# Optimization experiments

Measured on AMD Instinct MI355X. Metric: run time of the kernel, lower is better.

Reference implementation:

```python
import jax, jax.numpy as jnp
import numpy as np

N = 201        # nodes (100 visual + 100 audio + 1 text)
E = 40200      # directed edges (before self loops)
IN_CH = 1024
HD_CH = 1024
OUT_CH = 1024
HEADS = 8
C1 = HD_CH // HEADS   # 128 per-head channels, layer 1
C2 = OUT_CH // HEADS  # 128 per-head channels, layer 2
NUM_CLS = 2
NEG_SLOPE = 0.2


def setup_inputs() -> dict:
    key = jax.random.key(0)
    ks = jax.random.split(key, 16)

    def lin(k, out_d, in_d):
        return jax.random.normal(k, (out_d, in_d), jnp.float32) * (1.0 / np.sqrt(in_d))

    x = jax.random.normal(ks[0], (1, N, IN_CH), jnp.float32)
    edgeIds = jax.random.randint(ks[1], (2, E), 0, N, jnp.int64)
    return {
        "x": x,
        "edgeIds": edgeIds,
        # GATv2 layer 1
        "W1l": lin(ks[2], HEADS * C1, IN_CH), "b1l": jnp.zeros((HEADS * C1,), jnp.float32),
        "W1r": lin(ks[3], HEADS * C1, IN_CH), "b1r": jnp.zeros((HEADS * C1,), jnp.float32),
        "att1": jax.random.normal(ks[4], (HEADS, C1), jnp.float32) * (1.0 / np.sqrt(C1)),
        "bias1": jnp.zeros((HEADS * C1,), jnp.float32),
        # GATv2 layer 2
        "W2l": lin(ks[5], HEADS * C2, HD_CH), "b2l": jnp.zeros((HEADS * C2,), jnp.float32),
        "W2r": lin(ks[6], HEADS * C2, HD_CH), "b2r": jnp.zeros((HEADS * C2,), jnp.float32),
        "att2": jax.random.normal(ks[7], (HEADS, C2), jnp.float32) * (1.0 / np.sqrt(C2)),
        "bias2": jnp.zeros((HEADS * C2,), jnp.float32),
        # classifier
        "clfW": lin(ks[8], NUM_CLS, OUT_CH),
        "clfb": jnp.zeros((NUM_CLS,), jnp.float32),
    }


def _gatv2(x, src, dst, Wl, bl, Wr, br, att, bias, heads, ch):
    # x: [N, in_ch]; src/dst: [E'] (self loops included)
    n = x.shape[0]
    xl = (x @ Wl.T + bl).reshape(n, heads, ch)  # source transform
    xr = (x @ Wr.T + br).reshape(n, heads, ch)  # target transform
    # per-edge GATv2 score: a^T LeakyReLU(xl_j + xr_i)
    e = jax.nn.leaky_relu(xl[src] + xr[dst], NEG_SLOPE)   # [E', H, C]
    score = jnp.einsum("ehc,hc->eh", e, att)              # [E', H]
    # segment softmax over destination nodes (PyG convention)
    smax = jax.ops.segment_max(score, dst, num_segments=n)     # [N, H]
    ex = jnp.exp(score - smax[dst])                            # [E', H]
    denom = jax.ops.segment_sum(ex, dst, num_segments=n)       # [N, H]
    alpha = ex / (denom[dst] + 1e-16)                          # [E', H]
    out = jax.ops.segment_sum(alpha[:, :, None] * xl[src], dst, num_segments=n)
    return out.reshape(n, heads * ch) + bias


def reference(x, edgeIds, W1l, b1l, W1r, b1r, att1, bias1,
              W2l, b2l, W2r, b2r, att2, bias2, clfW, clfb):
    xs = jnp.squeeze(x, axis=0)  # [N, inChl]
    n = xs.shape[0]
    # add_self_loops=True (GATv2Conv default)
    loops = jnp.arange(n, dtype=edgeIds.dtype)
    src = jnp.concatenate([edgeIds[0], loops])
    dst = jnp.concatenate([edgeIds[1], loops])

    h = _gatv2(xs, src, dst, W1l, b1l, W1r, b1r, att1, bias1, HEADS, C1)
    h = jax.nn.relu(h)
    h = _gatv2(h, src, dst, W2l, b2l, W2r, b2r, att2, bias2, HEADS, C2)

    h = h[None]  # [1, N, outChl]
    # fuse_average: mean of visual (0:100), audio (100:200), text (node 200)
    avg = (jnp.mean(h[:, :100], axis=1) + jnp.mean(h[:, 100:200], axis=1) + h[:, 200]) / 3.0
    return avg @ clfW.T + clfb  # [1, numCls]
```

## Files before the change

kernel.cpp:

```cpp
#include <hip/hip_runtime.h>
#include <hip/hip_bf16.h>

#define HEADS 8
#define MPAD  208
#define KPAD  224
#define HROWS 112
#define NB    208

typedef __attribute__((ext_vector_type(8))) short short8v;
typedef __attribute__((ext_vector_type(4))) float float4v;

static __device__ __forceinline__ unsigned short f2bf(float f) {
    unsigned int u = __float_as_uint(f);
    u += 0x7FFF + ((u >> 16) & 1);
    return (unsigned short)(u >> 16);
}
static __device__ __forceinline__ float bf2f(unsigned short h) {
    return __uint_as_float(((unsigned int)h) << 16);
}

__global__ void k_mzero(int* M) {
    int i = blockIdx.x * 1024 + threadIdx.x;
    if (i < MPAD * KPAD) M[i] = 0;
}

__global__ void k_mcount(const int* __restrict__ srcA, const int* __restrict__ dstA,
                         int E, int N, int* __restrict__ M) {
    int e = blockIdx.x * 256 + threadIdx.x;
    if (e < E + N) {
        int d = (e < E) ? dstA[e] : (e - E);
        int s = (e < E) ? srcA[e] : (e - E);
        atomicAdd(&M[d * KPAD + s], 1);
    }
}

template<int MODE>
__global__ __launch_bounds__(256)
void k_gemm_mfma(const float* __restrict__ Xf, const unsigned short* __restrict__ Apl,
                 const float* __restrict__ Wl, const float* __restrict__ bl,
                 const float* __restrict__ Wr, const float* __restrict__ br,
                 unsigned short* __restrict__ outT) {
    __shared__ short lA[2 * HROWS * 40];
    __shared__ short lB[2 * 16 * 40];

    int tx = threadIdx.x;
    int panel = blockIdx.x >> 1;
    int half  = blockIdx.x & 1;
    int row0  = half * HROWS;
    int ntiles = half ? 6 : 7;
    int wv = tx >> 6, lane = tx & 63;
    int colpan = (panel & 63) * 16;
    const float* Wbase = (panel < 64) ? Wl : Wr;

    int gX[4], lX[4], rowv[4];
    #pragma unroll
    for (int j = 0; j < 4; ++j) {
        int idx = tx + 256 * j;
        if (MODE == 0) {
            int r = idx >> 3, seg = idx & 7;
            rowv[j] = row0 + r;
            gX[j] = (row0 + r) * 1024 + seg * 4;
            lX[j] = r * 40 + seg * 4;
        } else {
            int p = (idx >= 448);
            int rem = idx - p * 448;
            int r = rem >> 2, seg = rem & 3;
            rowv[j] = row0 + r;
            gX[j] = (p * MPAD + row0 + r) * 1024 + seg * 8;
            lX[j] = p * (HROWS * 40) + r * 40 + seg * 8;
        }
    }
    int wcol = tx >> 3, wseg = tx & 7;
    size_t goffW = (size_t)(colpan + wcol) * 1024 + wseg * 4;

    float4  af[4];
    short8v ap[4];
    float4  wreg;

    auto loadChunk = [&](int k0) {
        #pragma unroll
        for (int j = 0; j < 3; ++j) {
            if (MODE == 0) {
                af[j] = (rowv[j] < 201) ? *(const float4*)&Xf[gX[j] + k0]
                                        : make_float4(0.f, 0.f, 0.f, 0.f);
            } else {
                ap[j] = (rowv[j] < 201) ? *(const short8v*)&Apl[gX[j] + k0]
                                        : short8v{0,0,0,0,0,0,0,0};
            }
        }
        if (tx < 128) {
            if (MODE == 0) {
                af[3] = (rowv[3] < 201) ? *(const float4*)&Xf[gX[3] + k0]
                                        : make_float4(0.f, 0.f, 0.f, 0.f);
            } else {
                ap[3] = (rowv[3] < 201) ? *(const short8v*)&Apl[gX[3] + k0]
                                        : short8v{0,0,0,0,0,0,0,0};
            }
            wreg = *(const float4*)&Wbase[goffW + k0];
        }
    };
    auto storeSeg = [&](int j) {
        if (MODE == 0) {
            ushort4 hi, lo;
            hi.x = f2bf(af[j].x); lo.x = f2bf(af[j].x - bf2f(hi.x));
            hi.y = f2bf(af[j].y); lo.y = f2bf(af[j].y - bf2f(hi.y));
            hi.z = f2bf(af[j].z); lo.z = f2bf(af[j].z - bf2f(hi.z));
            hi.w = f2bf(af[j].w); lo.w = f2bf(af[j].w - bf2f(hi.w));
            *(ushort4*)&lA[lX[j]]              = hi;
            *(ushort4*)&lA[HROWS * 40 + lX[j]] = lo;
        } else {
            *(short8v*)&lA[lX[j]] = ap[j];
        }
    };
    auto storeChunk = [&]() {
        #pragma unroll
        for (int j = 0; j < 3; ++j) storeSeg(j);
        if (tx < 128) {
            storeSeg(3);
            ushort4 hi, lo;
            hi.x = f2bf(wreg.x); lo.x = f2bf(wreg.x - bf2f(hi.x));
            hi.y = f2bf(wreg.y); lo.y = f2bf(wreg.y - bf2f(hi.y));
            hi.z = f2bf(wreg.z); lo.z = f2bf(wreg.z - bf2f(hi.z));
            hi.w = f2bf(wreg.w); lo.w = f2bf(wreg.w - bf2f(hi.w));
            *(ushort4*)&lB[wcol * 40 + wseg * 4]        = hi;
            *(ushort4*)&lB[(16 + wcol) * 40 + wseg * 4] = lo;
        }
    };

    float4v acc[2] = {};
    int row16 = lane & 15;
    int k8    = (lane >> 4) * 8;

    loadChunk(0);
    for (int c = 0; c < 32; ++c) {
        __syncthreads();
        storeChunk();
        __syncthreads();
        if (c < 31) loadChunk((c + 1) * 32);
        short8v bh  = *(const short8v*)&lB[row16 * 40 + k8];
        short8v blo = *(const short8v*)&lB[(16 + row16) * 40 + k8];
        #pragma unroll
        for (int i = 0; i < 2; ++i) {
            int t = wv + 4 * i;
            if (t < ntiles) {
                short8v ah = *(const short8v*)&lA[(t * 16 + row16) * 40 + k8];
                short8v al = *(const short8v*)&lA[HROWS * 40 + (t * 16 + row16) * 40 + k8];
                acc[i] = __builtin_amdgcn_mfma_f32_16x16x32_bf16(ah, bh,  acc[i], 0, 0, 0);
                acc[i] = __builtin_amdgcn_mfma_f32_16x16x32_bf16(al, bh,  acc[i], 0, 0, 0);
                acc[i] = __builtin_amdgcn_mfma_f32_16x16x32_bf16(ah, blo, acc[i], 0, 0, 0);
            }
        }
    }

    int colg = panel * 16 + row16;
    float bias_val = ((panel < 64) ? bl : br)[colpan + row16];
    unsigned short* Th = outT;
    unsigned short* Tl = outT + (size_t)2048 * KPAD;
    #pragma unroll
    for (int i = 0; i < 2; ++i) {
        int t = wv + 4 * i;
        if (t < ntiles) {
            int rowb = row0 + t * 16 + (lane >> 4) * 4;
            ushort4 hi, lo;
            float v0 = acc[i][0] + bias_val, v1 = acc[i][1] + bias_val;
            float v2 = acc[i][2] + bias_val, v3 = acc[i][3] + bias_val;
            hi.x = f2bf(v0); lo.x = f2bf(v0 - bf2f(hi.x));
            hi.y = f2bf(v1); lo.y = f2bf(v1 - bf2f(hi.y));
            hi.z = f2bf(v2); lo.z = f2bf(v2 - bf2f(hi.z));
            hi.w = f2bf(v3); lo.w = f2bf(v3 - bf2f(hi.w));
            *(ushort4*)&Th[(size_t)colg * KPAD + rowb] = hi;
            *(ushort4*)&Tl[(size_t)colg * KPAD + rowb] = lo;
        }
    }
}

template<int LAYER1>
__global__ __launch_bounds__(256)
void k_score(const unsigned short* __restrict__ outT,
             const float* __restrict__ att, const float* __restrict__ bias,
             const int* __restrict__ M,
             unsigned short* __restrict__ hpl,
             const float* __restrict__ clfW, float* __restrict__ part) {
    __shared__ float xrt[8 * 128];
    __shared__ float a_l[128], a4_l[128];
    __shared__ float axr_l[8];
    __shared__ float Sm[8][256];
    __shared__ float smax_l[8], inv_l[8];
    __shared__ unsigned short aP[2][16][232];
    __shared__ float ps[4][2];

    int tx = threadIdx.x;
    int bid = blockIdx.x;
    int h = bid & 7, dt = bid >> 3;
    int w = tx >> 6, lane = tx & 63;
    const unsigned short* Th = outT;
    const unsigned short* Tl = outT + (size_t)2048 * KPAD;

    if (tx < 128) { float a = att[h * 128 + tx]; a_l[tx] = a; a4_l[tx] = 0.4f * a; }
    #pragma unroll
    for (int k = 0; k < 4; ++k) {
        int idx = tx + 256 * k;
        int c = idx >> 3, j = idx & 7;
        size_t o = (size_t)(1024 + h * 128 + c) * KPAD + dt * 8 + j;
        xrt[j * 128 + c] = bf2f(Th[o]) + bf2f(Tl[o]);
    }
    for (int k = tx; k < 2 * 8 * 232; k += 256) {
        int pl = k / (8 * 232), rem = k % (8 * 232);
        aP[pl][8 + rem / 232][rem % 232] = 0;
    }
    __syncthreads();
    if (tx < 64) {
        int j = tx >> 3, seg = tx & 7;
        float s = 0.f;
        for (int c = seg * 16; c < seg * 16 + 16; ++c) s += a_l[c] * xrt[j * 128 + c];
        s += __shfl_xor(s, 1, 64);
        s += __shfl_xor(s, 2, 64);
        s += __shfl_xor(s, 4, 64);
        if (seg == 0) axr_l[j] = s;
    }
    __syncthreads();

    float sc[8] = {};
    float axl = 0.f;
    {
        size_t base = (size_t)(h * 128) * KPAD + tx;
        for (int c = 0; c < 128; ++c) {
            size_t o = base + (size_t)c * KPAD;
            float xv = bf2f(Th[o]) + bf2f(Tl[o]);
            axl = fmaf(a_l[c], xv, axl);
            #pragma unroll
            for (int j = 0; j < 8; ++j) {
                float t0 = xv + xrt[j * 128 + c];
                sc[j] = fmaf(a4_l[c], fabsf(t0), sc[j]);
            }
        }
    }
    float cnt[8];
    #pragma unroll
    for (int j = 0; j < 8; ++j) {
        float c_ = 0.f;
        if (tx < KPAD) c_ = (float)M[(dt * 8 + j) * KPAD + tx];
        cnt[j] = c_;
        sc[j] = 0.6f * (axl + axr_l[j]) + sc[j];
        Sm[j][tx] = (c_ > 0.f) ? sc[j] : -__builtin_huge_valf();
    }
    __syncthreads();
    #pragma unroll
    for (int rr = 0; rr < 2; ++rr) {
        int j = w * 2 + rr;
        float v = fmaxf(fmaxf(Sm[j][lane], Sm[j][lane + 64]),
                        fmaxf(Sm[j][lane + 128], Sm[j][lane + 192]));
        #pragma unroll
        for (int hop = 1; hop <= 32; hop <<= 1) v = fmaxf(v, __shfl_xor(v, hop, 64));
        if (lane == 0) smax_l[j] = v;
    }
    __syncthreads();
    float pj[8];
    #pragma unroll
    for (int j = 0; j < 8; ++j) {
        float p = (cnt[j] > 0.f) ? cnt[j] * __expf(sc[j] - smax_l[j]) : 0.f;
        pj[j] = p;
        Sm[j][tx] = p;
    }
    __syncthreads();
    #pragma unroll
    for (int rr = 0; rr < 2; ++rr) {
        int j = w * 2 + rr;
        float v = Sm[j][lane] + Sm[j][lane + 64] + Sm[j][lane + 128] + Sm[j][lane + 192];
        #pragma unroll
        for (int hop = 1; hop <= 32; hop <<= 1) v += __shfl_xor(v, hop, 64);
        if (lane == 0) inv_l[j] = 1.f / (v + 1e-16f);
    }
    __syncthreads();
    if (tx < KPAD) {
        #pragma unroll
        for (int j = 0; j < 8; ++j) {
            float a = pj[j] * inv_l[j];
            unsigned short hi = f2bf(a);
            unsigned short lo = f2bf(a - bf2f(hi));
            aP[0][j][tx] = hi;
            aP[1][j][tx] = lo;
        }
    }
    __syncthreads();

    float4v acc[2] = {};
    int row16 = lane & 15;
    int k8 = (lane >> 4) * 8;
    for (int kc = 0; kc < 7; ++kc) {
        short8v Ah = *(const short8v*)&aP[0][row16][kc * 32 + k8];
        short8v Al = *(const short8v*)&aP[1][row16][kc * 32 + k8];
        #pragma unroll
        for (int cf = 0; cf < 2; ++cf) {
            int c_abs = h * 128 + w * 32 + cf * 16 + row16;
            size_t o = (size_t)c_abs * KPAD + kc * 32 + k8;
            short8v Bh = *(const short8v*)&Th[o];
            short8v Bl = *(const short8v*)&Tl[o];
            acc[cf] = __builtin_amdgcn_mfma_f32_16x16x32_bf16(Ah, Bh, acc[cf], 0, 0, 0);
            acc[cf] = __builtin_amdgcn_mfma_f32_16x16x32_bf16(Al, Bh, acc[cf], 0, 0, 0);
            acc[cf] = __builtin_amdgcn_mfma_f32_16x16x32_bf16(Ah, Bl, acc[cf], 0, 0, 0);
        }
    }

    int r = (lane >> 4) * 4;
    if (LAYER1) {
        if (r < 8) {
            #pragma unroll
            for (int cf = 0; cf < 2; ++cf) {
                int c_abs = h * 128 + w * 32 + cf * 16 + (lane & 15);
                float bv = bias[c_abs];
                #pragma unroll
                for (int j = 0; j < 4; ++j) {
                    int d = dt * 8 + r + j;
                    float val = fmaxf(acc[cf][j] + bv, 0.f);
                    unsigned short hi = f2bf(val);
                    unsigned short lo = f2bf(val - bf2f(hi));
                    hpl[(size_t)d * 1024 + c_abs]          = hi;
                    hpl[(size_t)(MPAD + d) * 1024 + c_abs] = lo;
                }
            }
        }
    } else {
        float p0 = 0.f, p1 = 0.f;
        if (r < 8) {
            #pragma unroll
            for (int cf = 0; cf < 2; ++cf) {
                int c_abs = h * 128 + w * 32 + cf * 16 + (lane & 15);
                float bv = bias[c_abs];
                float c0 = clfW[c_abs], c1 = clfW[1024 + c_abs];
                #pragma unroll
                for (int j = 0; j < 4; ++j) {
                    int d = dt * 8 + r + j;
                    if (d < 201) {
                        float val = acc[cf][j] + bv;
                        float wgt = (d == 200) ? (1.f / 3.f) : (1.f / 300.f);
                        p0 += wgt * val * c0;
                        p1 += wgt * val * c1;
                    }
                }
            }
        }
        #pragma unroll
        for (int hop = 1; hop <= 32; hop <<= 1) {
            p0 += __shfl_xor(p0, hop, 64);
            p1 += __shfl_xor(p1, hop, 64);
        }
        if (lane == 0) { ps[w][0] = p0; ps[w][1] = p1; }
        __syncthreads();
        if (tx == 0) {
            part[bid]      = ps[0][0] + ps[1][0] + ps[2][0] + ps[3][0];
            part[NB + bid] = ps[0][1] + ps[1][1] + ps[2][1] + ps[3][1];
        }
    }
}

__global__ __launch_bounds__(256)
void k_fin(const float* __restrict__ part, const float* __restrict__ clfb,
           float* __restrict__ outp) {
    int t = threadIdx.x;
    float s0 = (t < NB) ? part[t] : 0.f;
    float s1 = (t < NB) ? part[NB + t] : 0.f;
    __shared__ float r0[256], r1[256];
    r0[t] = s0; r1[t] = s1;
    __syncthreads();
    for (int off = 128; off > 0; off >>= 1) {
        if (t < off) { r0[t] += r0[t + off]; r1[t] += r1[t + off]; }
        __syncthreads();
    }
    if (t == 0) { outp[0] = r0[0] + clfb[0]; outp[1] = r0[0] * 0.f + r1[0] + clfb[1]; }
}

extern "C" void kernel_launch(void* const* d_in, const int* in_sizes, int n_in,
                              void* d_out, int out_size, void* d_ws, size_t ws_size,
                              hipStream_t stream) {
    const float* x     = (const float*)d_in[0];
    const int*   eids  = (const int*)d_in[1];
    const float* W1l   = (const float*)d_in[2];
    const float* b1l   = (const float*)d_in[3];
    const float* W1r   = (const float*)d_in[4];
    const float* b1r   = (const float*)d_in[5];
    const float* att1  = (const float*)d_in[6];
    const float* bias1 = (const float*)d_in[7];
    const float* W2l   = (const float*)d_in[8];
    const float* b2l   = (const float*)d_in[9];
    const float* W2r   = (const float*)d_in[10];
    const float* b2r   = (const float*)d_in[11];
    const float* att2  = (const float*)d_in[12];
    const float* bias2 = (const float*)d_in[13];
    const float* clfW  = (const float*)d_in[14];
    const float* clfb  = (const float*)d_in[15];
    float* outp = (float*)d_out;

    int N = in_sizes[0] / 1024;
    int E = in_sizes[1] / 2;
    int tot = E + N;

    char* wsp = (char*)d_ws;
    int* M = (int*)wsp;                         wsp += (size_t)MPAD * KPAD * 4;
    unsigned short* outT1 = (unsigned short*)wsp; wsp += (size_t)2 * 2048 * KPAD * 2;
    unsigned short* hpl   = (unsigned short*)wsp; wsp += (size_t)2 * MPAD * 1024 * 2;
    unsigned short* outT2 = (unsigned short*)wsp; wsp += (size_t)2 * 2048 * KPAD * 2;
    float* part = (float*)wsp;                   wsp += (size_t)2 * NB * 4;

    const int* srcA = eids;
    const int* dstA = eids + E;

    k_mzero <<<(MPAD * KPAD + 1023) / 1024, 1024, 0, stream>>>(M);
    k_mcount<<<(tot + 255) / 256, 256, 0, stream>>>(srcA, dstA, E, N, M);

    k_gemm_mfma<0><<<256, 256, 0, stream>>>(x, (const unsigned short*)nullptr,
                                            W1l, b1l, W1r, b1r, outT1);
    k_score<1><<<NB, 256, 0, stream>>>(outT1, att1, bias1, M,
                                       hpl, (const float*)nullptr, (float*)nullptr);
    k_gemm_mfma<1><<<256, 256, 0, stream>>>((const float*)nullptr, hpl,
                                            W2l, b2l, W2r, b2r, outT2);
    k_score<0><<<NB, 256, 0, stream>>>(outT2, att2, bias2, M,
                                       (unsigned short*)nullptr, clfW, part);
    k_fin<<<1, 256, 0, stream>>>(part, clfb, outp);
}
```

Before: 200.6 us.

## Fuse adjacency counting into score kernels and add row-major GEMM output copy

Removes the separate zeroing and edge-counting kernels. Each score block now scans the whole edge list and builds its own 8-row adjacency counts in shared memory with shared atomics. The GEMM also writes a second, node-major copy of its output, so the score kernel can read each node's per-head features as contiguous vector loads instead of strided column reads. The cost is redundant edge scans in every block (208 blocks × ~40k edges) and scattered scalar 2-byte stores in the GEMM epilogue.

```diff
diff --git a/kernel.cpp b/kernel.cpp
--- a/kernel.cpp
+++ b/kernel.cpp
@@ -19,27 +19,12 @@
     return __uint_as_float(((unsigned int)h) << 16);
 }
 
-__global__ void k_mzero(int* M) {
-    int i = blockIdx.x * 1024 + threadIdx.x;
-    if (i < MPAD * KPAD) M[i] = 0;
-}
-
-__global__ void k_mcount(const int* __restrict__ srcA, const int* __restrict__ dstA,
-                         int E, int N, int* __restrict__ M) {
-    int e = blockIdx.x * 256 + threadIdx.x;
-    if (e < E + N) {
-        int d = (e < E) ? dstA[e] : (e - E);
-        int s = (e < E) ? srcA[e] : (e - E);
-        atomicAdd(&M[d * KPAD + s], 1);
-    }
-}
-
 template<int MODE>
 __global__ __launch_bounds__(256)
 void k_gemm_mfma(const float* __restrict__ Xf, const unsigned short* __restrict__ Apl,
                  const float* __restrict__ Wl, const float* __restrict__ bl,
                  const float* __restrict__ Wr, const float* __restrict__ br,
-                 unsigned short* __restrict__ outT) {
+                 unsigned short* __restrict__ outT, unsigned short* __restrict__ outR) {
     __shared__ short lA[2 * HROWS * 40];
     __shared__ short lB[2 * 16 * 40];
 
@@ -156,6 +141,8 @@
     float bias_val = ((panel < 64) ? bl : br)[colpan + row16];
     unsigned short* Th = outT;
     unsigned short* Tl = outT + (size_t)2048 * KPAD;
+    unsigned short* Rh = outR;
+    unsigned short* Rl = outR + (size_t)KPAD * 2048;
     #pragma unroll
     for (int i = 0; i < 2; ++i) {
         int t = wv + 4 * i;
@@ -170,19 +157,29 @@
             hi.w = f2bf(v3); lo.w = f2bf(v3 - bf2f(hi.w));
             *(ushort4*)&Th[(size_t)colg * KPAD + rowb] = hi;
             *(ushort4*)&Tl[(size_t)colg * KPAD + rowb] = lo;
+            Rh[(size_t)(rowb + 0) * 2048 + colg] = hi.x;
+            Rh[(size_t)(rowb + 1) * 2048 + colg] = hi.y;
+            Rh[(size_t)(rowb + 2) * 2048 + colg] = hi.z;
+            Rh[(size_t)(rowb + 3) * 2048 + colg] = hi.w;
+            Rl[(size_t)(rowb + 0) * 2048 + colg] = lo.x;
+            Rl[(size_t)(rowb + 1) * 2048 + colg] = lo.y;
+            Rl[(size_t)(rowb + 2) * 2048 + colg] = lo.z;
+            Rl[(size_t)(rowb + 3) * 2048 + colg] = lo.w;
         }
     }
 }
 
 template<int LAYER1>
 __global__ __launch_bounds__(256)
-void k_score(const unsigned short* __restrict__ outT,
+void k_score(const unsigned short* __restrict__ T,
+             const unsigned short* __restrict__ R,
+             const int* __restrict__ eids, int E, int N,
              const float* __restrict__ att, const float* __restrict__ bias,
-             const int* __restrict__ M,
              unsigned short* __restrict__ hpl,
              const float* __restrict__ clfW, float* __restrict__ part) {
-    __shared__ float xrt[8 * 128];
-    __shared__ float a_l[128], a4_l[128];
+    __shared__ int   cntL[8][224];
+    __shared__ float xrt[128][8];
+    __shared__ float a2[128][2];
     __shared__ float axr_l[8];
     __shared__ float Sm[8][256];
     __shared__ float smax_l[8], inv_l[8];
@@ -191,28 +188,41 @@
 
     int tx = threadIdx.x;
     int bid = blockIdx.x;
-    int h = bid & 7, dt = bid >> 3;
+    int h = bid & 7, dt = bid >> 3, d0 = dt * 8;
     int w = tx >> 6, lane = tx & 63;
-    const unsigned short* Th = outT;
-    const unsigned short* Tl = outT + (size_t)2048 * KPAD;
-
-    if (tx < 128) { float a = att[h * 128 + tx]; a_l[tx] = a; a4_l[tx] = 0.4f * a; }
+    const unsigned short* Th = T;
+    const unsigned short* Tl = T + (size_t)2048 * KPAD;
+    const unsigned short* Rh = R;
+    const unsigned short* Rl = R + (size_t)KPAD * 2048;
+    const int* srcA = eids;
+    const int* dstA = eids + E;
+
+    for (int k = tx; k < 8 * 224; k += 256) ((int*)cntL)[k] = 0;
+    if (tx < 128) { float a = att[h * 128 + tx]; a2[tx][0] = a; a2[tx][1] = 0.4f * a; }
+    for (int k = tx; k < 2 * 8 * 232; k += 256) {
+        int pl = k / (8 * 232), rem = k % (8 * 232);
+        aP[pl][8 + rem / 232][rem % 232] = 0;
+    }
     #pragma unroll
     for (int k = 0; k < 4; ++k) {
         int idx = tx + 256 * k;
         int c = idx >> 3, j = idx & 7;
-        size_t o = (size_t)(1024 + h * 128 + c) * KPAD + dt * 8 + j;
-        xrt[j * 128 + c] = bf2f(Th[o]) + bf2f(Tl[o]);
-    }
-    for (int k = tx; k < 2 * 8 * 232; k += 256) {
-        int pl = k / (8 * 232), rem = k % (8 * 232);
-        aP[pl][8 + rem / 232][rem % 232] = 0;
-    }
-    __syncthreads();
+        size_t o = (size_t)(d0 + j) * 2048 + 1024 + h * 128 + c;
+        xrt[c][j] = bf2f(Rh[o]) + bf2f(Rl[o]);
+    }
+    __syncthreads();
+
+    for (int e = tx; e < E + N; e += 256) {
+        int d = (e < E) ? dstA[e] : (e - E);
+        if ((unsigned)(d - d0) < 8u) {
+            int s = (e < E) ? srcA[e] : (e - E);
+            atomicAdd(&cntL[d - d0][s], 1);
+        }
+    }
     if (tx < 64) {
         int j = tx >> 3, seg = tx & 7;
         float s = 0.f;
-        for (int c = seg * 16; c < seg * 16 + 16; ++c) s += a_l[c] * xrt[j * 128 + c];
+        for (int c = seg * 16; c < seg * 16 + 16; ++c) s += a2[c][0] * xrt[c][j];
         s += __shfl_xor(s, 1, 64);
         s += __shfl_xor(s, 2, 64);
         s += __shfl_xor(s, 4, 64);
@@ -222,24 +232,35 @@
 
     float sc[8] = {};
     float axl = 0.f;
-    {
-        size_t base = (size_t)(h * 128) * KPAD + tx;
-        for (int c = 0; c < 128; ++c) {
-            size_t o = base + (size_t)c * KPAD;
-            float xv = bf2f(Th[o]) + bf2f(Tl[o]);
-            axl = fmaf(a_l[c], xv, axl);
+    if (tx < KPAD) {
+        size_t base = (size_t)tx * 2048 + h * 128;
+        #pragma unroll 4
+        for (int q = 0; q < 16; ++q) {
+            short8v vh = *(const short8v*)&Rh[base + q * 8];
+            short8v vl = *(const short8v*)&Rl[base + q * 8];
             #pragma unroll
-            for (int j = 0; j < 8; ++j) {
-                float t0 = xv + xrt[j * 128 + c];
-                sc[j] = fmaf(a4_l[c], fabsf(t0), sc[j]);
+            for (int u = 0; u < 8; ++u) {
+                int c = q * 8 + u;
+                float xv = bf2f((unsigned short)vh[u]) + bf2f((unsigned short)vl[u]);
+                float2 av = *(const float2*)&a2[c][0];
+                axl = fmaf(av.x, xv, axl);
+                float4 xa = *(const float4*)&xrt[c][0];
+                float4 xb = *(const float4*)&xrt[c][4];
+                sc[0] = fmaf(av.y, fabsf(xv + xa.x), sc[0]);
+                sc[1] = fmaf(av.y, fabsf(xv + xa.y), sc[1]);
+                sc[2] = fmaf(av.y, fabsf(xv + xa.z), sc[2]);
+                sc[3] = fmaf(av.y, fabsf(xv + xa.w), sc[3]);
+                sc[4] = fmaf(av.y, fabsf(xv + xb.x), sc[4]);
+                sc[5] = fmaf(av.y, fabsf(xv + xb.y), sc[5]);
+                sc[6] = fmaf(av.y, fabsf(xv + xb.z), sc[6]);
+                sc[7] = fmaf(av.y, fabsf(xv + xb.w), sc[7]);
             }
         }
     }
     float cnt[8];
     #pragma unroll
     for (int j = 0; j < 8; ++j) {
-        float c_ = 0.f;
-        if (tx < KPAD) c_ = (float)M[(dt * 8 + j) * KPAD + tx];
+        float c_ = (tx < KPAD) ? (float)cntL[j][tx] : 0.f;
         cnt[j] = c_;
         sc[j] = 0.6f * (axl + axr_l[j]) + sc[j];
         Sm[j][tx] = (c_ > 0.f) ? sc[j] : -__builtin_huge_valf();
@@ -311,7 +332,7 @@
                 float bv = bias[c_abs];
                 #pragma unroll
                 for (int j = 0; j < 4; ++j) {
-                    int d = dt * 8 + r + j;
+                    int d = d0 + r + j;
                     float val = fmaxf(acc[cf][j] + bv, 0.f);
                     unsigned short hi = f2bf(val);
                     unsigned short lo = f2bf(val - bf2f(hi));
@@ -330,7 +351,7 @@
                 float c0 = clfW[c_abs], c1 = clfW[1024 + c_abs];
                 #pragma unroll
                 for (int j = 0; j < 4; ++j) {
-                    int d = dt * 8 + r + j;
+                    int d = d0 + r + j;
                     if (d < 201) {
                         float val = acc[cf][j] + bv;
                         float wgt = (d == 200) ? (1.f / 3.f) : (1.f / 300.f);
@@ -367,7 +388,7 @@
         if (t < off) { r0[t] += r0[t + off]; r1[t] += r1[t + off]; }
         __syncthreads();
     }
-    if (t == 0) { outp[0] = r0[0] + clfb[0]; outp[1] = r0[0] * 0.f + r1[0] + clfb[1]; }
+    if (t == 0) { outp[0] = r0[0] + clfb[0]; outp[1] = r1[0] + clfb[1]; }
 }
 
 extern "C" void kernel_launch(void* const* d_in, const int* in_sizes, int n_in,
@@ -393,28 +414,22 @@
 
     int N = in_sizes[0] / 1024;
     int E = in_sizes[1] / 2;
-    int tot = E + N;
 
     char* wsp = (char*)d_ws;
-    int* M = (int*)wsp;                         wsp += (size_t)MPAD * KPAD * 4;
-    unsigned short* outT1 = (unsigned short*)wsp; wsp += (size_t)2 * 2048 * KPAD * 2;
-    unsigned short* hpl   = (unsigned short*)wsp; wsp += (size_t)2 * MPAD * 1024 * 2;
-    unsigned short* outT2 = (unsigned short*)wsp; wsp += (size_t)2 * 2048 * KPAD * 2;
-    float* part = (float*)wsp;                   wsp += (size_t)2 * NB * 4;
-
-    const int* srcA = eids;
-    const int* dstA = eids + E;
-
-    k_mzero <<<(MPAD * KPAD + 1023) / 1024, 1024, 0, stream>>>(M);
-    k_mcount<<<(tot + 255) / 256, 256, 0, stream>>>(srcA, dstA, E, N, M);
+    unsigned short* T1  = (unsigned short*)wsp; wsp += (size_t)2 * 2048 * KPAD * 2;
+    unsigned short* R1  = (unsigned short*)wsp; wsp += (size_t)2 * KPAD * 2048 * 2;
+    unsigned short* hpl = (unsigned short*)wsp; wsp += (size_t)2 * MPAD * 1024 * 2;
+    unsigned short* T2  = (unsigned short*)wsp; wsp += (size_t)2 * 2048 * KPAD * 2;
+    unsigned short* R2  = (unsigned short*)wsp; wsp += (size_t)2 * KPAD * 2048 * 2;
+    float* part = (float*)wsp;                  wsp += (size_t)2 * NB * 4;
 
     k_gemm_mfma<0><<<256, 256, 0, stream>>>(x, (const unsigned short*)nullptr,
-                                            W1l, b1l, W1r, b1r, outT1);
-    k_score<1><<<NB, 256, 0, stream>>>(outT1, att1, bias1, M,
+                                            W1l, b1l, W1r, b1r, T1, R1);
+    k_score<1><<<NB, 256, 0, stream>>>(T1, R1, eids, E, N, att1, bias1,
                                        hpl, (const float*)nullptr, (float*)nullptr);
     k_gemm_mfma<1><<<256, 256, 0, stream>>>((const float*)nullptr, hpl,
-                                            W2l, b2l, W2r, b2r, outT2);
-    k_score<0><<<NB, 256, 0, stream>>>(outT2, att2, bias2, M,
+                                            W2l, b2l, W2r, b2r, T2, R2);
+    k_score<0><<<NB, 256, 0, stream>>>(T2, R2, eids, E, N, att2, bias2,
                                        (unsigned short*)nullptr, clfW, part);
     k_fin<<<1, 256, 0, stream>>>(part, clfb, outp);
 }
```

Measured after the change: 290.8 us. 1.45x slower.
